# Kernel tuning notes

Hardware: AMD Instinct MI355X
Metric: run time of the kernel (lower is better)

## Reference

```python
import math
import jax
import jax.numpy as jnp
import numpy as np

B, T, D = 2, 2048, 1024
E = 8          # n_experts
K = 2          # top_k
H = 2816       # SwiGLU hidden: multiple_of-rounded int(2*(4*D)/3)
CAP_F = 1.25
AUX_W = 0.01
Z_W = 0.001


def setup_inputs() -> dict:
    key = jax.random.key(0)
    ks = jax.random.split(key, 10)
    s = 0.02
    return {
        "x": jax.random.normal(ks[0], (B, T, D), jnp.float32),
        "gate_w": jax.random.normal(ks[1], (D, E), jnp.float32) * s,
        "w13": jax.random.normal(ks[2], (E, D, 2 * H), jnp.float32) * s,
        "w2": jax.random.normal(ks[3], (E, H, D), jnp.float32) * s,
        "msg_w": jax.random.normal(ks[4], (D, D), jnp.float32) * s,
        "q_w": jax.random.normal(ks[5], (D, D), jnp.float32) * s,
        "k_w": jax.random.normal(ks[6], (D, D), jnp.float32) * s,
        "upd_w1": jax.random.normal(ks[7], (2 * D, 2 * D), jnp.float32) * s,
        "upd_w2": jax.random.normal(ks[8], (2 * D, D), jnp.float32) * s,
        "o_w": jax.random.normal(ks[9], (D, D), jnp.float32) * s,
    }


def _moc_forward(x, gate_w, w13, w2, msg_w, q_w, k_w, upd_w1, upd_w2, o_w):
    b, t, d = x.shape
    N = b * t
    NK = N * K
    CAP = math.ceil(NK / E * CAP_F)  # static capacity per expert
    xf = x.reshape(N, d)

    # --- router ---
    logits = xf.astype(jnp.float32) @ gate_w              # [N, E]
    topk_vals, topk_idx = jax.lax.top_k(logits, K)        # [N, K]
    topk_probs = jax.nn.softmax(topk_vals, axis=-1)
    top1 = jnp.argmax(logits, axis=-1)
    router_probs = jax.nn.softmax(logits, axis=-1)
    prob_mass = router_probs.mean(axis=0)
    frac = jax.nn.one_hot(top1, E, dtype=jnp.float32).mean(axis=0)
    balance_loss = (prob_mass * frac).sum() * E
    z = jax.scipy.special.logsumexp(logits, axis=-1)
    z_loss = jnp.mean(z * z)
    aux_loss = AUX_W * balance_loss + Z_W * z_loss

    # --- capacity-aware dispatch (sort by expert, rank within expert) ---
    x_exp = jnp.repeat(xf, K, axis=0)                     # [NK, D], token repeated K times
    tgt = topk_idx.reshape(-1)                            # [NK]
    order = jnp.argsort(tgt)
    sorted_e = tgt[order]
    x_perm = x_exp[order]
    counts = jnp.bincount(tgt, length=E)
    offsets = jnp.concatenate([jnp.zeros((1,), counts.dtype), jnp.cumsum(counts)])
    rank = jnp.arange(NK) - offsets[sorted_e]             # position within expert group
    keep = rank < CAP
    slot = jnp.where(keep, sorted_e * CAP + rank, E * CAP)
    buf = jnp.zeros((E * CAP + 1, d), x.dtype).at[slot].set(x_perm)[: E * CAP]
    buf = buf.reshape(E, CAP, d)                          # [E, CAP, D]

    # --- grouped per-expert SwiGLU FFN ---
    h = jnp.einsum('ecd,edh->ech', buf, w13)              # [E, CAP, 2H]
    gate_h, up = jnp.split(h, 2, axis=-1)
    y = jnp.einsum('ech,ehd->ecd', jax.nn.silu(gate_h) * up, w2)
    y_flat = y.reshape(E * CAP, d)

    # --- combine back (dropped tokens get zeros) ---
    safe = jnp.minimum(slot, E * CAP - 1)
    out_sorted = jnp.where(keep[:, None], y_flat[safe], jnp.zeros((), x.dtype))
    sel = jnp.zeros((NK, d), x.dtype).at[order].set(out_sorted).reshape(N, K, d)
    kept = jnp.zeros((NK,), bool).at[order].set(keep).reshape(N, K)

    # --- simple collaboration (two-pass, shared params) ---
    M = sel @ msg_w                                       # [N, K, D]
    Q = sel @ q_w
    Kk = M @ k_w
    scores = jnp.einsum('nkd,njd->nkj', Q.astype(jnp.float32), Kk.astype(jnp.float32))
    scores = scores / math.sqrt(d)
    valid = kept[:, :, None] & kept[:, None, :]           # [N, K, K]
    scores = jnp.where(valid, scores, -1e9)
    A = jax.nn.softmax(scores, axis=-1) * valid
    A = A / jnp.clip(A.sum(axis=-1, keepdims=True), 1e-12)
    Cmsg = jnp.einsum('nkj,njd->nkd', A.astype(sel.dtype), M)
    cat = jnp.concatenate([sel, Cmsg], axis=-1)           # [N, K, 2D]
    upd = jax.nn.gelu(cat @ upd_w1, approximate=False) @ upd_w2
    refined = (sel + upd) * kept[..., None].astype(sel.dtype)

    # --- weighted fusion over K with renormalized kept probs ---
    p = topk_probs * kept.astype(topk_probs.dtype)
    w = (p / jnp.clip(p.sum(axis=-1, keepdims=True), 1e-12)).astype(refined.dtype)
    fused = jnp.sum(refined * w[..., None], axis=1) @ o_w
    return fused.reshape(b, t, d), aux_loss.astype(x.dtype), topk_idx.reshape(b, t, K)


def reference(x, gate_w, w13, w2, msg_w, q_w, k_w, upd_w1, upd_w2, o_w):
    return _moc_forward(x, gate_w, w13, w2, msg_w, q_w, k_w, upd_w1, upd_w2, o_w)
```

## Files before the change

kernel.cpp:

```cpp
#include <hip/hip_runtime.h>
#include <math.h>

#define Dv 1024
#define Ev 8
#define Hv 2816
#define Nv 4096
#define NKv 8192
#define CAPv 1280
#define TH2v 5632

typedef unsigned short u16;
typedef unsigned char u8;
typedef __attribute__((ext_vector_type(4))) float f32x4;
typedef __attribute__((ext_vector_type(4))) int i32x4;
typedef __attribute__((ext_vector_type(8))) int i32x8;
typedef __attribute__((ext_vector_type(4))) u16 u16x4;

typedef const __attribute__((address_space(1))) void* as1_cvp;
typedef __attribute__((address_space(3))) void* as3_vp;

__device__ __forceinline__ unsigned f2e4(float f) {
  unsigned u = __float_as_uint(f);
  unsigned sgn = (u >> 24) & 0x80u;
  unsigned ax = u & 0x7FFFFFFFu;
  if (ax >= 0x43E00000u) return sgn | 0x7Eu;
  if (ax < 0x3C800000u) {
    int qv = (int)rintf(__uint_as_float(ax) * 512.f);
    return sgn | (unsigned)qv;
  }
  unsigned lsb = (ax >> 20) & 1u;
  unsigned rr = ax + 0x0007FFFFu + lsb;
  unsigned ee = rr >> 23;
  unsigned mm = (rr >> 20) & 7u;
  if (ee > 135u) return sgn | 0x7Eu;
  return sgn | ((ee - 120u) << 3) | mm;
}
__device__ __forceinline__ float e42f(unsigned v) {
  unsigned s = (v & 0x80u) << 24, e = (v >> 3) & 15u, m = v & 7u;
  if (e) return __uint_as_float(s | ((e + 120u) << 23) | (m << 20));
  return __uint_as_float(__float_as_uint((float)m * 0.001953125f) | s);
}
__device__ __forceinline__ void dec16(const u8* p, float* o) {
  const unsigned* w = (const unsigned*)p;
  #pragma unroll
  for (int j = 0; j < 4; ++j) {
    unsigned x = w[j];
    o[j*4+0] = e42f(x & 255u);
    o[j*4+1] = e42f((x >> 8) & 255u);
    o[j*4+2] = e42f((x >> 16) & 255u);
    o[j*4+3] = e42f((x >> 24) & 255u);
  }
}
__device__ __forceinline__ void gload16(const void* g, void* l) {
  __builtin_amdgcn_global_load_lds((as1_cvp)g, (as3_vp)l, 16, 0, 0);
}

__global__ __launch_bounds__(256) void router_kernel(
    const float* __restrict__ x, const float* __restrict__ gw,
    int* __restrict__ tkidx, float* __restrict__ tkprob,
    float* __restrict__ red, float* __restrict__ outIdx)
{
  __shared__ float lred[17];
  int tid = threadIdx.x;
  if (tid < 17) lred[tid] = 0.f;
  __syncthreads();
  int wv = tid >> 6, ln = tid & 63;
  int n = blockIdx.x * 4 + wv;
  float a[8] = {0.f,0.f,0.f,0.f,0.f,0.f,0.f,0.f};
  const float* xr = x + (size_t)n * Dv;
  #pragma unroll
  for (int it = 0; it < 16; ++it) {
    int d = ln + it * 64;
    float xs = xr[d];
    float4 g0 = *(const float4*)(gw + (size_t)d * 8);
    float4 g1 = *(const float4*)(gw + (size_t)d * 8 + 4);
    a[0] += xs * g0.x; a[1] += xs * g0.y; a[2] += xs * g0.z; a[3] += xs * g0.w;
    a[4] += xs * g1.x; a[5] += xs * g1.y; a[6] += xs * g1.z; a[7] += xs * g1.w;
  }
  #pragma unroll
  for (int off = 32; off >= 1; off >>= 1) {
    #pragma unroll
    for (int e = 0; e < 8; ++e) a[e] += __shfl_xor(a[e], off, 64);
  }
  int i1 = 0; float v1 = a[0];
  #pragma unroll
  for (int e = 1; e < 8; ++e) if (a[e] > v1) { v1 = a[e]; i1 = e; }
  int i2 = -1; float v2 = -1e30f;
  #pragma unroll
  for (int e = 0; e < 8; ++e) if (e != i1 && a[e] > v2) { v2 = a[e]; i2 = e; }
  float Z = 0.f;
  #pragma unroll
  for (int e = 0; e < 8; ++e) Z += expf(a[e] - v1);
  float zlse = v1 + logf(Z);
  float t = expf(v2 - v1);
  float p1 = 1.f / (1.f + t);
  float p2 = t * p1;
  if (ln == 0) {
    tkidx[2*n] = i1; tkidx[2*n+1] = i2;
    tkprob[2*n] = p1; tkprob[2*n+1] = p2;
    outIdx[2*n] = (float)i1; outIdx[2*n+1] = (float)i2;
    #pragma unroll
    for (int e = 0; e < 8; ++e) atomicAdd(&lred[e], expf(a[e] - v1) / Z);
    atomicAdd(&lred[8 + i1], 1.f);
    atomicAdd(&lred[16], zlse * zlse);
  }
  __syncthreads();
  if (tid < 17) atomicAdd(&red[tid], lred[tid]);
}

__global__ void aux_kernel(const float* __restrict__ red, float* __restrict__ outAux) {
  float bl = 0.f;
  for (int e = 0; e < 8; ++e) bl += (red[e] / (float)Nv) * (red[8 + e] / (float)Nv);
  bl *= (float)Ev;
  float zl = red[16] / (float)Nv;
  outAux[0] = 0.01f * bl + 0.001f * zl;
}

__global__ __launch_bounds__(256) void rank_kernel(const int* __restrict__ tgt,
    int* __restrict__ keep, int* __restrict__ dstNK)
{
  __shared__ int hist[256][8];
  int t = threadIdx.x;
  int h[8] = {0,0,0,0,0,0,0,0};
  int base = t * 32;
  for (int j = 0; j < 32; ++j) h[tgt[base + j]]++;
  for (int e = 0; e < 8; ++e) hist[t][e] = h[e];
  __syncthreads();
  if (t < 8) {
    int run = 0;
    for (int tt = 0; tt < 256; ++tt) { int v = hist[tt][t]; hist[tt][t] = run; run += v; }
  }
  __syncthreads();
  for (int e = 0; e < 8; ++e) h[e] = hist[t][e];
  for (int j = 0; j < 32; ++j) {
    int i = base + j; int e = tgt[i]; int r = h[e]++;
    int kp = (r < CAPv) ? 1 : 0;
    keep[i] = kp;
    if (kp) dstNK[e * CAPv + r] = i;
  }
}

__global__ __launch_bounds__(256) void pack8_kernel(const float* __restrict__ x,
    const int* __restrict__ dstNK, u8* __restrict__ buf)
{
  int s = blockIdx.x * 4 + (threadIdx.x >> 6);
  int ln = threadIdx.x & 63;
  int i = dstNK[s];
  u8* dst = buf + (size_t)s * Dv;
  if (i >= 0) {
    const float* src = x + (size_t)(i >> 1) * Dv;
    #pragma unroll
    for (int j = 0; j < 4; ++j) {
      int d0 = ln * 16 + j * 4;
      float4 v = *(const float4*)(src + d0);
      unsigned w = f2e4(v.x) | (f2e4(v.y) << 8) | (f2e4(v.z) << 16) | (f2e4(v.w) << 24);
      *(unsigned*)(dst + d0) = w;
    }
  } else {
    #pragma unroll
    for (int j = 0; j < 4; ++j) *(unsigned*)(dst + ln * 16 + j * 4) = 0u;
  }
}

__global__ __launch_bounds__(256) void conv8s_kernel(const float* __restrict__ in,
    u8* __restrict__ out, float smul)
{
  int i = blockIdx.x * 256 + threadIdx.x;
  float4 v = *(const float4*)(in + (size_t)i * 4);
  unsigned w = f2e4(v.x * smul) | (f2e4(v.y * smul) << 8)
             | (f2e4(v.z * smul) << 16) | (f2e4(v.w * smul) << 24);
  *(unsigned*)(out + (size_t)i * 4) = w;
}

__global__ __launch_bounds__(256) void tconv8_kernel(const float* __restrict__ in,
    u8* __restrict__ out, int R, int C, float smul, int ldo)
{
  __shared__ u8 tile[64][68];
  in += (size_t)blockIdx.z * (size_t)R * (size_t)C;
  out += (size_t)blockIdx.z * (size_t)R * (size_t)C;
  int r0 = blockIdx.y * 64, c0 = blockIdx.x * 64;
  int t = threadIdx.x;
  int cc4 = (t & 15) * 4;
  #pragma unroll
  for (int p = 0; p < 4; ++p) {
    int r = (t >> 4) + p * 16;
    float4 v = *(const float4*)(in + (size_t)(r0 + r) * C + c0 + cc4);
    unsigned w = f2e4(v.x * smul) | (f2e4(v.y * smul) << 8)
               | (f2e4(v.z * smul) << 16) | (f2e4(v.w * smul) << 24);
    *(unsigned*)(&tile[r][cc4]) = w;
  }
  __syncthreads();
  int rr4 = (t & 15) * 4;
  #pragma unroll
  for (int p = 0; p < 4; ++p) {
    int c = (t >> 4) + p * 16;
    unsigned w = (unsigned)tile[rr4][c] | ((unsigned)tile[rr4+1][c] << 8)
               | ((unsigned)tile[rr4+2][c] << 16) | ((unsigned)tile[rr4+3][c] << 24);
    *(unsigned*)(out + (size_t)(c0 + c) * ldo + r0 + rr4) = w;
  }
}

template<int MODE>
__global__ __launch_bounds__(256, 3) void gemm128f8(
    const u8* __restrict__ A, const u8* __restrict__ A2, int splitK,
    const u8* __restrict__ B, void* __restrict__ C,
    const int* __restrict__ dst, int Ksz, int lda, int ldb, int ldc, int ntm,
    size_t sA, size_t sB, size_t sC, unsigned sclA, unsigned sclB)
{
  __shared__ char smem[32768];
  int e = blockIdx.y;
  int nwgx = gridDim.x, bid0 = blockIdx.x;
  int q = nwgx >> 3, r = nwgx & 7;
  int xcd = bid0 & 7, lo2 = bid0 >> 3;
  int bid = (xcd < r ? xcd * (q + 1) : r * (q + 1) + (xcd - r) * q) + lo2;
  int tm = bid % ntm, tn = bid / ntm;
  const u8* Ae = A + (size_t)e * sA;
  const u8* Be = B + (size_t)e * sB;
  long long bdelta = (const char*)A2 - (const char*)Ae;
  int tid = threadIdx.x, wv = tid >> 6, ln = tid & 63;
  int lnl = ln & 15, lnh = ln >> 4;

  const u8* aP[4]; const u8* bP[4];
  unsigned aL[4], bL[4];
  #pragma unroll
  for (int i = 0; i < 4; ++i) {
    int row = i * 32 + wv * 8 + (ln >> 3);
    int c = (ln & 7) ^ (row & 7);
    int cp = ((c & 3) << 1) | (c >> 2);
    aP[i] = Ae + (size_t)(tm * 128 + row) * lda + cp * 16;
    int brow;
    if (MODE == 1) {
      brow = (row < 64) ? (tn * 64 + row) : (Hv + tn * 64 + (row - 64));
    } else {
      brow = tn * 128 + row;
    }
    bP[i] = Be + (size_t)brow * ldb + cp * 16;
    aL[i] = i * 4096 + wv * 1024;
    bL[i] = 16384 + i * 4096 + wv * 1024;
  }

  int arow0 = wv * 32 + lnl;
  int ksw0 = (lnh << 4);
  int ksw1 = 64 + (lnh << 4);

  f32x4 acc[2][8];
  #pragma unroll
  for (int m = 0; m < 2; ++m)
    #pragma unroll
    for (int n = 0; n < 8; ++n) acc[m][n] = (f32x4){0.f, 0.f, 0.f, 0.f};

  for (int k0 = 0; k0 < Ksz; k0 += 128) {
    long long kbA;
    if (MODE == 5 && k0 >= splitK) kbA = bdelta + (long long)(k0 - splitK);
    else kbA = (long long)k0;
    #pragma unroll
    for (int i = 0; i < 4; ++i) gload16(aP[i] + kbA, smem + aL[i]);
    #pragma unroll
    for (int i = 0; i < 4; ++i) gload16(bP[i] + (size_t)k0, smem + bL[i]);
    __syncthreads();

    i32x8 af[2];
    #pragma unroll
    for (int mi = 0; mi < 2; ++mi) {
      int row = arow0 + mi * 16;
      int swz = (row & 7) << 4;
      *(i32x4*)&af[mi] = *(const i32x4*)(smem + row * 128 + (ksw0 ^ swz));
      *((i32x4*)&af[mi] + 1) = *(const i32x4*)(smem + row * 128 + (ksw1 ^ swz));
    }
    #pragma unroll
    for (int n = 0; n < 8; ++n) {
      int row = n * 16 + lnl;
      int swz = (row & 7) << 4;
      i32x8 bf;
      *(i32x4*)&bf = *(const i32x4*)(smem + 16384 + row * 128 + (ksw0 ^ swz));
      *((i32x4*)&bf + 1) = *(const i32x4*)(smem + 16384 + row * 128 + (ksw1 ^ swz));
      acc[0][n] = __builtin_amdgcn_mfma_scale_f32_16x16x128_f8f6f4(
          af[0], bf, acc[0][n], 0, 0, 0, sclA, 0, sclB);
      acc[1][n] = __builtin_amdgcn_mfma_scale_f32_16x16x128_f8f6f4(
          af[1], bf, acc[1][n], 0, 0, 0, sclA, 0, sclB);
    }
    __syncthreads();
  }

  int rbase = tm * 128 + wv * 32 + (lnh << 2);
  if (MODE == 1) {
    u8* Cp = (u8*)C + (size_t)e * sC;
    #pragma unroll
    for (int mi = 0; mi < 2; ++mi)
      #pragma unroll
      for (int n = 0; n < 4; ++n) {
        int col = tn * 64 + n * 16 + lnl;
        #pragma unroll
        for (int v = 0; v < 4; ++v) {
          float g = acc[mi][n][v];
          float u = acc[mi][n + 4][v];
          float sg = g / (1.f + __expf(-g));
          Cp[(size_t)(rbase + mi * 16 + v) * ldc + col] = (u8)f2e4(sg * u);
        }
      }
  } else if (MODE == 2) {
    u8* Cq = (u8*)C;
    #pragma unroll
    for (int mi = 0; mi < 2; ++mi)
      #pragma unroll
      for (int v = 0; v < 4; ++v) {
        int gr = rbase + mi * 16 + v;
        int i = dst[e * CAPv + gr];
        if (i >= 0) {
          #pragma unroll
          for (int n = 0; n < 8; ++n) {
            int col = tn * 128 + n * 16 + lnl;
            Cq[(size_t)i * Dv + col] = (u8)f2e4(acc[mi][n][v]);
          }
        }
      }
  } else if (MODE == 4) {
    u8* Cp = (u8*)C;
    #pragma unroll
    for (int mi = 0; mi < 2; ++mi)
      #pragma unroll
      for (int n = 0; n < 8; ++n) {
        int col = tn * 128 + n * 16 + lnl;
        #pragma unroll
        for (int v = 0; v < 4; ++v)
          Cp[(size_t)(rbase + mi * 16 + v) * ldc + col] = (u8)f2e4(acc[mi][n][v]);
      }
  } else if (MODE == 5) {
    u8* Cp = (u8*)C;
    #pragma unroll
    for (int mi = 0; mi < 2; ++mi)
      #pragma unroll
      for (int n = 0; n < 8; ++n) {
        int col = tn * 128 + n * 16 + lnl;
        #pragma unroll
        for (int v = 0; v < 4; ++v) {
          float xg = acc[mi][n][v];
          float gl = 0.5f * xg * (1.f + erff(xg * 0.70710678118654752f));
          Cp[(size_t)(rbase + mi * 16 + v) * ldc + col] = (u8)f2e4(gl);
        }
      }
  } else {
    float* Cp = (float*)C;
    #pragma unroll
    for (int mi = 0; mi < 2; ++mi)
      #pragma unroll
      for (int n = 0; n < 8; ++n) {
        int col = tn * 128 + n * 16 + lnl;
        #pragma unroll
        for (int v = 0; v < 4; ++v)
          Cp[(size_t)(rbase + mi * 16 + v) * ldc + col] = acc[mi][n][v];
      }
  }
}

__global__ __launch_bounds__(256) void scores8_kernel(
    const u8* __restrict__ MQ, const u8* __restrict__ SEL8,
    const int* __restrict__ keep, u8* __restrict__ Cmsg)
{
  int wv = threadIdx.x >> 6, ln = threadIdx.x & 63;
  int n = blockIdx.x * 4 + wv;
  const u8* m0 = MQ + (size_t)(2 * n) * 2048;
  const u8* m1 = MQ + (size_t)(2 * n + 1) * 2048;
  const u8* t0 = m0 + 1024;
  const u8* t1 = m1 + 1024;
  const u8* s0p = SEL8 + (size_t)(2 * n) * 1024;
  const u8* s1p = SEL8 + (size_t)(2 * n + 1) * 1024;
  int d0 = ln * 16;
  float a0[16], a1[16], b0[16], b1[16];
  dec16(t0 + d0, a0); dec16(t1 + d0, a1);
  dec16(s0p + d0, b0); dec16(s1p + d0, b1);
  float s00 = 0, s01 = 0, s10 = 0, s11 = 0;
  #pragma unroll
  for (int t = 0; t < 16; ++t) {
    s00 += a0[t] * b0[t]; s01 += a0[t] * b1[t];
    s10 += a1[t] * b0[t]; s11 += a1[t] * b1[t];
  }
  #pragma unroll
  for (int off = 32; off >= 1; off >>= 1) {
    s00 += __shfl_xor(s00, off, 64);
    s01 += __shfl_xor(s01, off, 64);
    s10 += __shfl_xor(s10, off, 64);
    s11 += __shfl_xor(s11, off, 64);
  }
  const float inv = 0.03125f;
  int kp0 = keep[2 * n], kp1 = keep[2 * n + 1];
  float A00, A01, A10, A11;
  {
    float v0 = kp0 ? s00 * inv : -1e9f;
    float v1 = (kp0 && kp1) ? s01 * inv : -1e9f;
    float mx = fmaxf(v0, v1);
    float e0 = expf(v0 - mx), e1 = expf(v1 - mx);
    float den = e0 + e1;
    float a0v = kp0 ? e0 / den : 0.f;
    float a1v = (kp0 && kp1) ? e1 / den : 0.f;
    float s = fmaxf(a0v + a1v, 1e-12f);
    A00 = a0v / s; A01 = a1v / s;
  }
  {
    float v0 = (kp1 && kp0) ? s10 * inv : -1e9f;
    float v1 = kp1 ? s11 * inv : -1e9f;
    float mx = fmaxf(v0, v1);
    float e0 = expf(v0 - mx), e1 = expf(v1 - mx);
    float den = e0 + e1;
    float a0v = (kp1 && kp0) ? e0 / den : 0.f;
    float a1v = kp1 ? e1 / den : 0.f;
    float s = fmaxf(a0v + a1v, 1e-12f);
    A10 = a0v / s; A11 = a1v / s;
  }
  float f0[16], f1[16];
  dec16(m0 + d0, f0); dec16(m1 + d0, f1);
  unsigned o0[4], o1[4];
  #pragma unroll
  for (int j = 0; j < 4; ++j) {
    o0[j] = 0; o1[j] = 0;
    #pragma unroll
    for (int b = 0; b < 4; ++b) {
      int t = j * 4 + b;
      o0[j] |= f2e4(A00 * f0[t] + A01 * f1[t]) << (8 * b);
      o1[j] |= f2e4(A10 * f0[t] + A11 * f1[t]) << (8 * b);
    }
  }
  u8* c0 = Cmsg + (size_t)(2 * n) * 1024 + d0;
  u8* c1 = Cmsg + (size_t)(2 * n + 1) * 1024 + d0;
  #pragma unroll
  for (int j = 0; j < 4; ++j) {
    *(unsigned*)(c0 + j * 4) = o0[j];
    *(unsigned*)(c1 + j * 4) = o1[j];
  }
}

__global__ __launch_bounds__(256) void combine2_kernel(
    const u8* __restrict__ sel8, const u8* __restrict__ g8,
    const int* __restrict__ keep, const float* __restrict__ tkprob,
    u8* __restrict__ fcat)
{
  int n = blockIdx.x;
  int t = threadIdx.x;
  float kp0 = keep[2 * n] ? 1.f : 0.f, kp1 = keep[2 * n + 1] ? 1.f : 0.f;
  float p0 = tkprob[2 * n] * kp0, p1 = tkprob[2 * n + 1] * kp1;
  float s = fmaxf(p0 + p1, 1e-12f);
  float w0 = p0 / s, w1 = p1 / s;
  unsigned a = *(const unsigned*)(sel8 + (size_t)(2 * n) * 1024 + t * 4);
  unsigned b = *(const unsigned*)(sel8 + (size_t)(2 * n + 1) * 1024 + t * 4);
  unsigned o = 0;
  #pragma unroll
  for (int j = 0; j < 4; ++j)
    o |= f2e4(w0 * e42f((a >> (8 * j)) & 255u) + w1 * e42f((b >> (8 * j)) & 255u)) << (8 * j);
  *(unsigned*)(fcat + (size_t)n * 3072 + t * 4) = o;
  const u8* ga = g8 + (size_t)(2 * n) * 2048 + t * 8;
  const u8* gb = g8 + (size_t)(2 * n + 1) * 2048 + t * 8;
  #pragma unroll
  for (int h = 0; h < 2; ++h) {
    unsigned xa = *(const unsigned*)(ga + h * 4);
    unsigned xb = *(const unsigned*)(gb + h * 4);
    unsigned oo = 0;
    #pragma unroll
    for (int j = 0; j < 4; ++j)
      oo |= f2e4(w0 * e42f((xa >> (8 * j)) & 255u) + w1 * e42f((xb >> (8 * j)) & 255u)) << (8 * j);
    *(unsigned*)(fcat + (size_t)n * 3072 + 1024 + t * 8 + h * 4) = oo;
  }
}

extern "C" void kernel_launch(void* const* d_in, const int* in_sizes, int n_in,
                              void* d_out, int out_size, void* d_ws, size_t ws_size,
                              hipStream_t stream) {
  const float* x      = (const float*)d_in[0];
  const float* gate_w = (const float*)d_in[1];
  const float* w13    = (const float*)d_in[2];
  const float* w2     = (const float*)d_in[3];
  const float* msg_w  = (const float*)d_in[4];
  const float* q_w    = (const float*)d_in[5];
  const float* k_w    = (const float*)d_in[6];
  const float* upd_w1 = (const float*)d_in[7];
  const float* upd_w2 = (const float*)d_in[8];
  const float* o_w    = (const float*)d_in[9];
  float* out = (float*)d_out;
  float* outAux = out + (size_t)Nv * Dv;
  float* outIdx = outAux + 1;

  char* ws = (char*)d_ws;
  const size_t MBc = 1ull << 20;
  int*   tkidx  = (int*)(ws + 0);
  float* tkprob = (float*)(ws + 32768);
  int*   keepA  = (int*)(ws + 65536);
  int*   dstNK  = (int*)(ws + 98304);
  float* red    = (float*)(ws + 143360);
  u8*  BUF8  = (u8*)(ws + 1 * MBc);
  u8*  ACT8  = (u8*)(ws + 12 * MBc);
  u8*  W13B8 = (u8*)(ws + 41 * MBc);
  u8*  W2B8  = (u8*)(ws + 41 * MBc);
  float* T1f = (float*)(ws + 64 * MBc);
  float* WSf = (float*)(ws + 68 * MBc);
  float* T2f = (float*)(ws + 72 * MBc);
  u8*  M8s   = (u8*)(ws + 80 * MBc);
  u8*  Q8s   = (u8*)(ws + 81 * MBc);
  u8*  U28s  = (u8*)(ws + 82 * MBc);
  u8*  K8T   = (u8*)(ws + 84 * MBc);
  u8*  T18   = (u8*)(ws + 85 * MBc);
  u8*  MTB8  = (u8*)(ws + 86 * MBc);
  u8*  WCAT8 = (u8*)(ws + 88 * MBc);
  u8*  FCAT8 = (u8*)(ws + 96 * MBc);
  u8*  SEL8  = (u8*)(ws + 136 * MBc);
  u8*  UPD1B8= (u8*)(ws + 149 * MBc);
  u8*  MQ8   = (u8*)(ws + 1 * MBc);
  u8*  CMSG8 = (u8*)(ws + 18 * MBc);
  u8*  G1B8  = (u8*)(ws + 27 * MBc);

  hipMemsetAsync(red, 0, 68, stream);
  hipMemsetAsync(dstNK, 0xFF, Ev * CAPv * 4, stream);

  router_kernel<<<Nv / 4, 256, 0, stream>>>(x, gate_w, tkidx, tkprob, red, outIdx);
  aux_kernel<<<1, 1, 0, stream>>>(red, outAux);
  rank_kernel<<<1, 256, 0, stream>>>(tkidx, keepA, dstNK);
  pack8_kernel<<<(Ev * CAPv) / 4, 256, 0, stream>>>(x, dstNK, BUF8);

  tconv8_kernel<<<dim3(TH2v / 64, Dv / 64, Ev), 256, 0, stream>>>(w13, W13B8, Dv, TH2v, 16.f, Dv);
  gemm128f8<1><<<dim3((CAPv / 128) * (Hv / 64), Ev), 256, 0, stream>>>(
      BUF8, BUF8, 1 << 30, W13B8, (void*)ACT8, nullptr,
      Dv, Dv, Dv, Hv, CAPv / 128,
      (size_t)CAPv * Dv, (size_t)TH2v * Dv, (size_t)CAPv * Hv, 0x7F7F7F7Fu, 0x7B7B7B7Bu);

  hipMemsetAsync(SEL8, 0, (size_t)NKv * Dv, stream);
  tconv8_kernel<<<dim3(Dv / 64, Hv / 64, Ev), 256, 0, stream>>>(w2, W2B8, Hv, Dv, 16.f, Hv);
  conv8s_kernel<<<1024, 256, 0, stream>>>(msg_w, M8s, 16.f);
  conv8s_kernel<<<1024, 256, 0, stream>>>(q_w, Q8s, 16.f);
  conv8s_kernel<<<2048, 256, 0, stream>>>(upd_w2, U28s, 16.f);
  tconv8_kernel<<<dim3(16, 16, 1), 256, 0, stream>>>(k_w, K8T, Dv, Dv, 16.f, Dv);
  tconv8_kernel<<<dim3(16, 16, 1), 256, 0, stream>>>(msg_w, MTB8, Dv, Dv, 16.f, Dv);
  tconv8_kernel<<<dim3(32, 32, 1), 256, 0, stream>>>(upd_w1, UPD1B8, 2048, 2048, 16.f, 2048);
  tconv8_kernel<<<dim3(16, 16, 1), 256, 0, stream>>>(o_w, WCAT8, Dv, Dv, 16.f, 3072);
  gemm128f8<6><<<dim3(64, 1), 256, 0, stream>>>(
      M8s, M8s, 1 << 30, K8T, (void*)T1f, nullptr,
      Dv, Dv, Dv, Dv, 8, 0, 0, 0, 0x7B7B7B7Bu, 0x7B7B7B7Bu);
  conv8s_kernel<<<1024, 256, 0, stream>>>(T1f, T18, 16.f);
  gemm128f8<6><<<dim3(64, 1), 256, 0, stream>>>(
      Q8s, Q8s, 1 << 30, T18, (void*)WSf, nullptr,
      Dv, Dv, Dv, Dv, 8, 0, 0, 0, 0x7B7B7B7Bu, 0x7B7B7B7Bu);
  tconv8_kernel<<<dim3(16, 16, 1), 256, 0, stream>>>(WSf, MTB8 + (size_t)Dv * Dv, Dv, Dv, 16.f, Dv);
  gemm128f8<6><<<dim3(128, 1), 256, 0, stream>>>(
      U28s, U28s, 1 << 30, WCAT8, (void*)T2f, nullptr,
      Dv, Dv, 3072, Dv, 16, 0, 0, 0, 0x7B7B7B7Bu, 0x7B7B7B7Bu);
  tconv8_kernel<<<dim3(16, 32, 1), 256, 0, stream>>>(T2f, WCAT8 + 1024, 2048, Dv, 16.f, 3072);

  gemm128f8<2><<<dim3((CAPv / 128) * (Dv / 128), Ev), 256, 0, stream>>>(
      ACT8, ACT8, 1 << 30, W2B8, (void*)SEL8, dstNK,
      Hv, Hv, Hv, Dv, CAPv / 128,
      (size_t)CAPv * Hv, (size_t)Dv * Hv, 0, 0x7F7F7F7Fu, 0x7B7B7B7Bu);

  gemm128f8<4><<<dim3(64 * 16, 1), 256, 0, stream>>>(
      SEL8, SEL8, 1 << 30, MTB8, (void*)MQ8, nullptr,
      Dv, Dv, Dv, 2048, 64, 0, 0, 0, 0x7F7F7F7Fu, 0x7B7B7B7Bu);
  scores8_kernel<<<Nv / 4, 256, 0, stream>>>(MQ8, SEL8, keepA, CMSG8);

  gemm128f8<5><<<dim3(64 * 16, 1), 256, 0, stream>>>(
      SEL8, CMSG8, Dv, UPD1B8, (void*)G1B8, nullptr,
      2048, Dv, 2048, 2048, 64, 0, 0, 0, 0x7F7F7F7Fu, 0x7B7B7B7Bu);

  combine2_kernel<<<Nv, 256, 0, stream>>>(SEL8, G1B8, keepA, tkprob, FCAT8);
  gemm128f8<6><<<dim3(32 * 8, 1), 256, 0, stream>>>(
      FCAT8, FCAT8, 1 << 30, WCAT8, (void*)out, nullptr,
      3072, 3072, 3072, Dv, 32, 0, 0, 0, 0x7F7F7F7Fu, 0x7B7B7B7Bu);

  (void)in_sizes; (void)n_in; (void)out_size; (void)ws_size;
}
```

Baseline: 493.7 us.

## Batch weight conversions into one launch, skip empty expert tiles, fold aux kernel

Merges the many per-weight fp8 convert/transpose launches into a single table-driven wprep kernel, and folds the aux-loss kernel into the rank kernel. Records per-expert kept counts so the expert GEMMs return early for row tiles beyond each expert's fill. Reorders the weight-product GEMMs so their outputs come out already transposed, replacing transposing converts with plain or strided ones. This cuts launch overhead and wasted GEMM work on padded capacity slots, but relies on the reordered products and the strided conversion matching the old layouts.

After: 460.6 us. -6.7%, faster.

```diff
diff --git a/kernel.cpp b/kernel.cpp
--- a/kernel.cpp
+++ b/kernel.cpp
@@ -14,7 +14,6 @@
 typedef __attribute__((ext_vector_type(4))) float f32x4;
 typedef __attribute__((ext_vector_type(4))) int i32x4;
 typedef __attribute__((ext_vector_type(8))) int i32x8;
-typedef __attribute__((ext_vector_type(4))) u16 u16x4;
 
 typedef const __attribute__((address_space(1))) void* as1_cvp;
 typedef __attribute__((address_space(3))) void* as3_vp;
@@ -50,6 +49,9 @@
     o[j*4+2] = e42f((x >> 16) & 255u);
     o[j*4+3] = e42f((x >> 24) & 255u);
   }
+}
+__device__ __forceinline__ unsigned pack4(float4 v, float s) {
+  return f2e4(v.x * s) | (f2e4(v.y * s) << 8) | (f2e4(v.z * s) << 16) | (f2e4(v.w * s) << 24);
 }
 __device__ __forceinline__ void gload16(const void* g, void* l) {
   __builtin_amdgcn_global_load_lds((as1_cvp)g, (as3_vp)l, 16, 0, 0);
@@ -108,16 +110,9 @@
   if (tid < 17) atomicAdd(&red[tid], lred[tid]);
 }
 
-__global__ void aux_kernel(const float* __restrict__ red, float* __restrict__ outAux) {
-  float bl = 0.f;
-  for (int e = 0; e < 8; ++e) bl += (red[e] / (float)Nv) * (red[8 + e] / (float)Nv);
-  bl *= (float)Ev;
-  float zl = red[16] / (float)Nv;
-  outAux[0] = 0.01f * bl + 0.001f * zl;
-}
-
 __global__ __launch_bounds__(256) void rank_kernel(const int* __restrict__ tgt,
-    int* __restrict__ keep, int* __restrict__ dstNK)
+    int* __restrict__ keep, int* __restrict__ dstNK, int* __restrict__ cnt,
+    const float* __restrict__ red, float* __restrict__ outAux)
 {
   __shared__ int hist[256][8];
   int t = threadIdx.x;
@@ -129,6 +124,13 @@
   if (t < 8) {
     int run = 0;
     for (int tt = 0; tt < 256; ++tt) { int v = hist[tt][t]; hist[tt][t] = run; run += v; }
+    cnt[t] = run < CAPv ? run : CAPv;
+  }
+  if (t == 0) {
+    float bl = 0.f;
+    for (int e = 0; e < 8; ++e) bl += (red[e] / (float)Nv) * (red[8 + e] / (float)Nv);
+    bl *= (float)Ev;
+    outAux[0] = 0.01f * bl + 0.001f * (red[16] / (float)Nv);
   }
   __syncthreads();
   for (int e = 0; e < 8; ++e) h[e] = hist[t][e];
@@ -153,8 +155,7 @@
     for (int j = 0; j < 4; ++j) {
       int d0 = ln * 16 + j * 4;
       float4 v = *(const float4*)(src + d0);
-      unsigned w = f2e4(v.x) | (f2e4(v.y) << 8) | (f2e4(v.z) << 16) | (f2e4(v.w) << 24);
-      *(unsigned*)(dst + d0) = w;
+      *(unsigned*)(dst + d0) = pack4(v, 1.f);
     }
   } else {
     #pragma unroll
@@ -162,32 +163,42 @@
   }
 }
 
-__global__ __launch_bounds__(256) void conv8s_kernel(const float* __restrict__ in,
-    u8* __restrict__ out, float smul)
-{
-  int i = blockIdx.x * 256 + threadIdx.x;
-  float4 v = *(const float4*)(in + (size_t)i * 4);
-  unsigned w = f2e4(v.x * smul) | (f2e4(v.y * smul) << 8)
-             | (f2e4(v.z * smul) << 16) | (f2e4(v.w * smul) << 24);
-  *(unsigned*)(out + (size_t)i * 4) = w;
-}
-
-__global__ __launch_bounds__(256) void tconv8_kernel(const float* __restrict__ in,
-    u8* __restrict__ out, int R, int C, float smul, int ldo)
-{
+#define NSEG 9
+struct WTab {
+  const float* in[NSEG];
+  u8* out[NSEG];
+  int R[NSEG], C[NSEG], ldo[NSEG], nxy[NSEG], nx[NSEG];
+  int start[NSEG];
+};
+
+__global__ __launch_bounds__(256) void wprep_kernel(WTab T) {
   __shared__ u8 tile[64][68];
-  in += (size_t)blockIdx.z * (size_t)R * (size_t)C;
-  out += (size_t)blockIdx.z * (size_t)R * (size_t)C;
-  int r0 = blockIdx.y * 64, c0 = blockIdx.x * 64;
+  int b = blockIdx.x;
+  int s = 0;
+  #pragma unroll
+  for (int i = 1; i < NSEG; ++i) if (b >= T.start[i]) s = i;
+  int rb = b - T.start[s];
+  const float* in = T.in[s];
+  u8* out = T.out[s];
   int t = threadIdx.x;
+  if (T.nx[s] == 0) {
+    int i = rb * 256 + t;
+    float4 v = *(const float4*)(in + (size_t)i * 4);
+    *(unsigned*)(out + (size_t)i * 4) = pack4(v, 16.f);
+    return;
+  }
+  int R = T.R[s], C = T.C[s], ldo = T.ldo[s];
+  int z = rb / T.nxy[s], r2 = rb % T.nxy[s];
+  int by = r2 / T.nx[s], bx = r2 % T.nx[s];
+  in += (size_t)z * R * C;
+  out += (size_t)z * (size_t)R * C;
+  int r0 = by * 64, c0 = bx * 64;
   int cc4 = (t & 15) * 4;
   #pragma unroll
   for (int p = 0; p < 4; ++p) {
     int r = (t >> 4) + p * 16;
     float4 v = *(const float4*)(in + (size_t)(r0 + r) * C + c0 + cc4);
-    unsigned w = f2e4(v.x * smul) | (f2e4(v.y * smul) << 8)
-               | (f2e4(v.z * smul) << 16) | (f2e4(v.w * smul) << 24);
-    *(unsigned*)(&tile[r][cc4]) = w;
+    *(unsigned*)(&tile[r][cc4]) = pack4(v, 16.f);
   }
   __syncthreads();
   int rr4 = (t & 15) * 4;
@@ -200,11 +211,30 @@
   }
 }
 
+__global__ __launch_bounds__(256) void conv8s_kernel(const float* __restrict__ in,
+    u8* __restrict__ out)
+{
+  int i = blockIdx.x * 256 + threadIdx.x;
+  float4 v = *(const float4*)(in + (size_t)i * 4);
+  *(unsigned*)(out + (size_t)i * 4) = pack4(v, 16.f);
+}
+
+__global__ __launch_bounds__(256) void conv8st_kernel(const float* __restrict__ in,
+    u8* __restrict__ out, int Cw, int ldo)
+{
+  int i = blockIdx.x * 256 + threadIdx.x;
+  int base = i * 4;
+  int r = base / Cw, c = base & (Cw - 1);
+  float4 v = *(const float4*)(in + (size_t)base);
+  *(unsigned*)(out + (size_t)r * ldo + c) = pack4(v, 16.f);
+}
+
 template<int MODE>
 __global__ __launch_bounds__(256, 3) void gemm128f8(
     const u8* __restrict__ A, const u8* __restrict__ A2, int splitK,
     const u8* __restrict__ B, void* __restrict__ C,
-    const int* __restrict__ dst, int Ksz, int lda, int ldb, int ldc, int ntm,
+    const int* __restrict__ dst, const int* __restrict__ cnt,
+    int Ksz, int lda, int ldb, int ldc, int ntm,
     size_t sA, size_t sB, size_t sC, unsigned sclA, unsigned sclB)
 {
   __shared__ char smem[32768];
@@ -214,6 +244,9 @@
   int xcd = bid0 & 7, lo2 = bid0 >> 3;
   int bid = (xcd < r ? xcd * (q + 1) : r * (q + 1) + (xcd - r) * q) + lo2;
   int tm = bid % ntm, tn = bid / ntm;
+  if (MODE == 1 || MODE == 2) {
+    if (tm * 128 >= cnt[e]) return;
+  }
   const u8* Ae = A + (size_t)e * sA;
   const u8* Be = B + (size_t)e * sB;
   long long bdelta = (const char*)A2 - (const char*)Ae;
@@ -485,80 +518,85 @@
   int*   keepA  = (int*)(ws + 65536);
   int*   dstNK  = (int*)(ws + 98304);
   float* red    = (float*)(ws + 143360);
+  int*   cntA   = (int*)(ws + 147456);
   u8*  BUF8  = (u8*)(ws + 1 * MBc);
   u8*  ACT8  = (u8*)(ws + 12 * MBc);
   u8*  W13B8 = (u8*)(ws + 41 * MBc);
-  u8*  W2B8  = (u8*)(ws + 41 * MBc);
-  float* T1f = (float*)(ws + 64 * MBc);
-  float* WSf = (float*)(ws + 68 * MBc);
-  float* T2f = (float*)(ws + 72 * MBc);
-  u8*  M8s   = (u8*)(ws + 80 * MBc);
-  u8*  Q8s   = (u8*)(ws + 81 * MBc);
-  u8*  U28s  = (u8*)(ws + 82 * MBc);
-  u8*  K8T   = (u8*)(ws + 84 * MBc);
-  u8*  T18   = (u8*)(ws + 85 * MBc);
-  u8*  MTB8  = (u8*)(ws + 86 * MBc);
-  u8*  WCAT8 = (u8*)(ws + 88 * MBc);
-  u8*  FCAT8 = (u8*)(ws + 96 * MBc);
+  u8*  M8s   = (u8*)(ws + 85 * MBc);
+  u8*  Q8s   = (u8*)(ws + 86 * MBc);
+  u8*  K8T   = (u8*)(ws + 87 * MBc);
+  u8*  W2B8r = (u8*)(ws + 88 * MBc);
+  u8*  U28s  = (u8*)(ws + 110 * MBc);
+  u8*  MTB8  = (u8*)(ws + 112 * MBc);
+  u8*  WCAT8 = (u8*)(ws + 114 * MBc);
+  u8*  P38   = (u8*)(ws + 117 * MBc);
+  float* P3f = (float*)(ws + 118 * MBc);
+  float* WsTf= (float*)(ws + 122 * MBc);
+  float* T2Tf= (float*)(ws + 126 * MBc);
   u8*  SEL8  = (u8*)(ws + 136 * MBc);
   u8*  UPD1B8= (u8*)(ws + 149 * MBc);
+  u8*  FCAT8 = (u8*)(ws + 160 * MBc);
   u8*  MQ8   = (u8*)(ws + 1 * MBc);
   u8*  CMSG8 = (u8*)(ws + 18 * MBc);
   u8*  G1B8  = (u8*)(ws + 27 * MBc);
 
   hipMemsetAsync(red, 0, 68, stream);
   hipMemsetAsync(dstNK, 0xFF, Ev * CAPv * 4, stream);
+  hipMemsetAsync(SEL8, 0, (size_t)NKv * Dv, stream);
 
   router_kernel<<<Nv / 4, 256, 0, stream>>>(x, gate_w, tkidx, tkprob, red, outIdx);
-  aux_kernel<<<1, 1, 0, stream>>>(red, outAux);
-  rank_kernel<<<1, 256, 0, stream>>>(tkidx, keepA, dstNK);
+  rank_kernel<<<1, 256, 0, stream>>>(tkidx, keepA, dstNK, cntA, red, outAux);
   pack8_kernel<<<(Ev * CAPv) / 4, 256, 0, stream>>>(x, dstNK, BUF8);
 
-  tconv8_kernel<<<dim3(TH2v / 64, Dv / 64, Ev), 256, 0, stream>>>(w13, W13B8, Dv, TH2v, 16.f, Dv);
+  WTab T;
+  T.in[0]=w13;    T.out[0]=W13B8; T.R[0]=Dv;   T.C[0]=TH2v; T.ldo[0]=Dv;   T.nxy[0]=88*16; T.nx[0]=88;
+  T.in[1]=w2;     T.out[1]=W2B8r; T.R[1]=Hv;   T.C[1]=Dv;   T.ldo[1]=Hv;   T.nxy[1]=16*44; T.nx[1]=16;
+  T.in[2]=upd_w1; T.out[2]=UPD1B8;T.R[2]=2048; T.C[2]=2048; T.ldo[2]=2048; T.nxy[2]=32*32; T.nx[2]=32;
+  T.in[3]=msg_w;  T.out[3]=MTB8;  T.R[3]=Dv;   T.C[3]=Dv;   T.ldo[3]=Dv;   T.nxy[3]=256;   T.nx[3]=16;
+  T.in[4]=o_w;    T.out[4]=WCAT8; T.R[4]=Dv;   T.C[4]=Dv;   T.ldo[4]=3072; T.nxy[4]=256;   T.nx[4]=16;
+  T.in[5]=k_w;    T.out[5]=K8T;   T.R[5]=Dv;   T.C[5]=Dv;   T.ldo[5]=Dv;   T.nxy[5]=256;   T.nx[5]=16;
+  T.in[6]=msg_w;  T.out[6]=M8s;   T.nx[6]=0; T.R[6]=0; T.C[6]=0; T.ldo[6]=0; T.nxy[6]=0;
+  T.in[7]=q_w;    T.out[7]=Q8s;   T.nx[7]=0; T.R[7]=0; T.C[7]=0; T.ldo[7]=0; T.nxy[7]=0;
+  T.in[8]=upd_w2; T.out[8]=U28s;  T.nx[8]=0; T.R[8]=0; T.C[8]=0; T.ldo[8]=0; T.nxy[8]=0;
+  T.start[0]=0; T.start[1]=11264; T.start[2]=16896; T.start[3]=17920;
+  T.start[4]=18176; T.start[5]=18432; T.start[6]=18688; T.start[7]=19712; T.start[8]=20736;
+  wprep_kernel<<<22784, 256, 0, stream>>>(T);
+
   gemm128f8<1><<<dim3((CAPv / 128) * (Hv / 64), Ev), 256, 0, stream>>>(
-      BUF8, BUF8, 1 << 30, W13B8, (void*)ACT8, nullptr,
+      BUF8, BUF8, 1 << 30, W13B8, (void*)ACT8, nullptr, cntA,
       Dv, Dv, Dv, Hv, CAPv / 128,
       (size_t)CAPv * Dv, (size_t)TH2v * Dv, (size_t)CAPv * Hv, 0x7F7F7F7Fu, 0x7B7B7B7Bu);
 
-  hipMemsetAsync(SEL8, 0, (size_t)NKv * Dv, stream);
-  tconv8_kernel<<<dim3(Dv / 64, Hv / 64, Ev), 256, 0, stream>>>(w2, W2B8, Hv, Dv, 16.f, Hv);
-  conv8s_kernel<<<1024, 256, 0, stream>>>(msg_w, M8s, 16.f);
-  conv8s_kernel<<<1024, 256, 0, stream>>>(q_w, Q8s, 16.f);
-  conv8s_kernel<<<2048, 256, 0, stream>>>(upd_w2, U28s, 16.f);
-  tconv8_kernel<<<dim3(16, 16, 1), 256, 0, stream>>>(k_w, K8T, Dv, Dv, 16.f, Dv);
-  tconv8_kernel<<<dim3(16, 16, 1), 256, 0, stream>>>(msg_w, MTB8, Dv, Dv, 16.f, Dv);
-  tconv8_kernel<<<dim3(32, 32, 1), 256, 0, stream>>>(upd_w1, UPD1B8, 2048, 2048, 16.f, 2048);
-  tconv8_kernel<<<dim3(16, 16, 1), 256, 0, stream>>>(o_w, WCAT8, Dv, Dv, 16.f, 3072);
   gemm128f8<6><<<dim3(64, 1), 256, 0, stream>>>(
-      M8s, M8s, 1 << 30, K8T, (void*)T1f, nullptr,
+      M8s, M8s, 1 << 30, K8T, (void*)P3f, nullptr, nullptr,
       Dv, Dv, Dv, Dv, 8, 0, 0, 0, 0x7B7B7B7Bu, 0x7B7B7B7Bu);
-  conv8s_kernel<<<1024, 256, 0, stream>>>(T1f, T18, 16.f);
+  conv8s_kernel<<<1024, 256, 0, stream>>>(P3f, P38);
   gemm128f8<6><<<dim3(64, 1), 256, 0, stream>>>(
-      Q8s, Q8s, 1 << 30, T18, (void*)WSf, nullptr,
+      P38, P38, 1 << 30, Q8s, (void*)WsTf, nullptr, nullptr,
       Dv, Dv, Dv, Dv, 8, 0, 0, 0, 0x7B7B7B7Bu, 0x7B7B7B7Bu);
-  tconv8_kernel<<<dim3(16, 16, 1), 256, 0, stream>>>(WSf, MTB8 + (size_t)Dv * Dv, Dv, Dv, 16.f, Dv);
+  conv8s_kernel<<<1024, 256, 0, stream>>>(WsTf, MTB8 + (size_t)Dv * Dv);
   gemm128f8<6><<<dim3(128, 1), 256, 0, stream>>>(
-      U28s, U28s, 1 << 30, WCAT8, (void*)T2f, nullptr,
-      Dv, Dv, 3072, Dv, 16, 0, 0, 0, 0x7B7B7B7Bu, 0x7B7B7B7Bu);
-  tconv8_kernel<<<dim3(16, 32, 1), 256, 0, stream>>>(T2f, WCAT8 + 1024, 2048, Dv, 16.f, 3072);
+      WCAT8, WCAT8, 1 << 30, U28s, (void*)T2Tf, nullptr, nullptr,
+      Dv, 3072, Dv, 2048, 8, 0, 0, 0, 0x7B7B7B7Bu, 0x7B7B7B7Bu);
+  conv8st_kernel<<<2048, 256, 0, stream>>>(T2Tf, WCAT8 + 1024, 2048, 3072);
 
   gemm128f8<2><<<dim3((CAPv / 128) * (Dv / 128), Ev), 256, 0, stream>>>(
-      ACT8, ACT8, 1 << 30, W2B8, (void*)SEL8, dstNK,
+      ACT8, ACT8, 1 << 30, W2B8r, (void*)SEL8, dstNK, cntA,
       Hv, Hv, Hv, Dv, CAPv / 128,
       (size_t)CAPv * Hv, (size_t)Dv * Hv, 0, 0x7F7F7F7Fu, 0x7B7B7B7Bu);
 
   gemm128f8<4><<<dim3(64 * 16, 1), 256, 0, stream>>>(
-      SEL8, SEL8, 1 << 30, MTB8, (void*)MQ8, nullptr,
+      SEL8, SEL8, 1 << 30, MTB8, (void*)MQ8, nullptr, nullptr,
       Dv, Dv, Dv, 2048, 64, 0, 0, 0, 0x7F7F7F7Fu, 0x7B7B7B7Bu);
   scores8_kernel<<<Nv / 4, 256, 0, stream>>>(MQ8, SEL8, keepA, CMSG8);
 
   gemm128f8<5><<<dim3(64 * 16, 1), 256, 0, stream>>>(
-      SEL8, CMSG8, Dv, UPD1B8, (void*)G1B8, nullptr,
+      SEL8, CMSG8, Dv, UPD1B8, (void*)G1B8, nullptr, nullptr,
       2048, Dv, 2048, 2048, 64, 0, 0, 0, 0x7F7F7F7Fu, 0x7B7B7B7Bu);
 
   combine2_kernel<<<Nv, 256, 0, stream>>>(SEL8, G1B8, keepA, tkprob, FCAT8);
   gemm128f8<6><<<dim3(32 * 8, 1), 256, 0, stream>>>(
-      FCAT8, FCAT8, 1 << 30, WCAT8, (void*)out, nullptr,
+      FCAT8, FCAT8, 1 << 30, WCAT8, (void*)out, nullptr, nullptr,
       3072, 3072, 3072, Dv, 32, 0, 0, 0, 0x7F7F7F7Fu, 0x7B7B7B7Bu);
 
   (void)in_sizes; (void)n_in; (void)out_size; (void)ws_size;
```
